# Kernel tuning notes

Measured on AMD Instinct MI355X. Metric: run time of the kernel, lower is better.

Reference implementation:

```python
import jax, jax.numpy as jnp
import numpy as np

B = 65536
A_CH, S_CH, D_CH = 64, 256, 256
IN_CH = A_CH + S_CH + D_CH   # 576
MID = 32
OUT_CH = 4 * S_CH            # 1024
R_IN = IN_CH + S_CH          # 832

def _xavier(key, fan_in, fan_out):
    lim = np.sqrt(6.0 / (fan_in + fan_out)).astype(np.float32)
    return jax.random.uniform(key, (fan_in, fan_out), jnp.float32, -lim, lim)

def setup_inputs() -> dict:
    key = jax.random.key(0)
    ks = jax.random.split(key, 8)
    return {
        "prev_h": jax.random.normal(ks[0], (B, S_CH), jnp.float32),
        "prev_c": jax.random.normal(ks[1], (B, S_CH), jnp.float32),
        "action": jax.random.normal(ks[2], (B, A_CH), jnp.float32),
        "dynamics": jax.random.normal(ks[3], (B, D_CH), jnp.float32),
        "W1": _xavier(ks[4], IN_CH, MID),
        "b1": jnp.zeros((MID,), jnp.float32),
        "W2": _xavier(ks[5], MID, OUT_CH),
        "b2": jnp.zeros((OUT_CH,), jnp.float32),
        "Wr": _xavier(ks[6], R_IN, 1),
        "br": jnp.zeros((1,), jnp.float32),
    }

def reference(prev_h, prev_c, action, dynamics, W1, b1, W2, b2, Wr, br):
    # concat order matches torch: [dynamics, action, prev_h] -> [B, 576]
    x = jnp.concatenate([dynamics, action, prev_h], axis=1)
    h1 = jnp.tanh(x @ W1 + b1)            # fc1: tanh activation, [B, 32]
    g = h1 @ W2 + b2                       # fc2: no activation, [B, 4*S]
    act_i, act_f, hat_c, act_o = jnp.split(g, 4, axis=1)
    act_i = jax.nn.sigmoid(act_i)
    act_f = jax.nn.sigmoid(act_f)
    hat_c = jnp.tanh(hat_c)
    act_o = jax.nn.sigmoid(act_o)
    next_c = act_f * prev_c + act_i * hat_c
    next_h = act_o * jnp.tanh(next_c)
    xr = jnp.concatenate([x, next_h], axis=1)  # [B, 832]
    reward = jnp.tanh(xr @ Wr + br)            # [B, 1]
    return next_h, next_c, reward
```

## Files before the change

### kernel.cpp

```cpp
#include <hip/hip_runtime.h>
#include <hip/hip_bf16.h>

typedef float f32x4 __attribute__((ext_vector_type(4)));
typedef short bf16x8 __attribute__((ext_vector_type(8)));
typedef float float4v __attribute__((ext_vector_type(4)));

#define W2T_OFF (48 * 576)
#define H1_OFF (W2T_OFF + 32 * 1024)

__device__ __forceinline__ short f2bf(float f) {
  __bf16 b = (__bf16)f;
  return __builtin_bit_cast(short, b);
}
__device__ __forceinline__ uint pack2(float a, float b) {
  return (uint)(unsigned short)f2bf(a) | ((uint)(unsigned short)f2bf(b) << 16);
}
__device__ __forceinline__ float fast_sigmoid(float x) {
  return __builtin_amdgcn_rcpf(1.f + __expf(-x));
}
__device__ __forceinline__ float fast_tanh(float x) {
  float e = __expf(2.f * x);
  return 1.f - 2.f * __builtin_amdgcn_rcpf(e + 1.f);
}
__device__ __forceinline__ float4v ld16(const float* p) {
  float4v r;
  asm volatile("global_load_dwordx4 %0, %1, off" : "=v"(r) : "v"(p));
  return r;
}

__global__ __launch_bounds__(256) void prep_weights(
    const float* __restrict__ W1, const float* __restrict__ W2,
    const float* __restrict__ Wr, short* __restrict__ ws)
{
  int i = blockIdx.x * 256 + threadIdx.x;
  if (i < 48 * 576) {
    int n = i / 576;
    int k = i - n * 576;
    float v = 0.f;
    if (n < 32) v = W1[k * 32 + n];
    else if (n == 32) v = Wr[k];
    int phys = n * 576 + ((((k >> 3) ^ (n & 7)) << 3) | (k & 7));
    ws[phys] = f2bf(v);
  } else {
    int j = i - 48 * 576;
    if (j < 32 * 1024) {
      int n = j >> 5;
      int k = j & 31;
      ws[W2T_OFF + j] = f2bf(W2[k * 1024 + n]);
    }
  }
}

__global__ __launch_bounds__(512, 4) void fc1_kernel(
    const float* __restrict__ prev_h, const float* __restrict__ action,
    const float* __restrict__ dynamics, const float* __restrict__ b1,
    const short* __restrict__ wsw, short* __restrict__ h1out,
    float* __restrict__ rdot)
{
  __shared__ short wlds[48 * 576];

  const int t = threadIdx.x;
  #pragma unroll
  for (int i = 0; i < 7; ++i) {
    int off = i * 8192 + t * 16;
    if (off < 55296) {
      __builtin_amdgcn_global_load_lds(
          (const __attribute__((address_space(1))) void*)((const char*)wsw + off),
          (__attribute__((address_space(3))) void*)((char*)wlds + off), 16, 0, 0);
    }
  }
  __syncthreads();

  const int wid = t >> 6, lane = t & 63, lg = lane >> 4, ln = lane & 15;
  const int lnx = ln & 7;
  const int rowA = blockIdx.x * 128 + wid * 16 + ln;
  const int kb = 8 * lg;

  const float* dynp = dynamics + rowA * 256 + kb;
  const float* actp = action   + rowA * 64  + kb;
  const float* hp   = prev_h   + rowA * 256 + kb;

  auto asrc = [&](int j) -> const float* {
    return (j < 8) ? (dynp + 32 * j)
         : (j < 10) ? (actp + 32 * j - 256)
                    : (hp + 32 * j - 320);
  };

  f32x4 acc0 = {0.f,0.f,0.f,0.f};
  f32x4 acc1 = {0.f,0.f,0.f,0.f};
  f32x4 acc2 = {0.f,0.f,0.f,0.f};

  float4v ab[6][2];
  #pragma unroll
  for (int j = 0; j < 6; ++j) {
    const float* p = asrc(j);
    ab[j][0] = ld16(p);
    ab[j][1] = ld16(p + 4);
  }

#define FC1_STEP(J, S, IMM)                                                  \
  {                                                                          \
    asm volatile("s_waitcnt vmcnt(" #IMM ")");                               \
    __builtin_amdgcn_sched_barrier(0);                                       \
    float4v v0 = ab[S][0], v1 = ab[S][1];                                    \
    bf16x8 a;                                                                \
    a[0]=f2bf(v0.x); a[1]=f2bf(v0.y); a[2]=f2bf(v0.z); a[3]=f2bf(v0.w);      \
    a[4]=f2bf(v1.x); a[5]=f2bf(v1.y); a[6]=f2bf(v1.z); a[7]=f2bf(v1.w);      \
    const int uo = ((4 * (J) + lg) ^ lnx) << 3;                              \
    bf16x8 bA = *(const bf16x8*)&wlds[ln * 576 + uo];                        \
    bf16x8 bB = *(const bf16x8*)&wlds[(ln + 16) * 576 + uo];                 \
    bf16x8 bC = *(const bf16x8*)&wlds[(ln + 32) * 576 + uo];                 \
    acc0 = __builtin_amdgcn_mfma_f32_16x16x32_bf16(bA, a, acc0, 0, 0, 0);    \
    acc1 = __builtin_amdgcn_mfma_f32_16x16x32_bf16(bB, a, acc1, 0, 0, 0);    \
    acc2 = __builtin_amdgcn_mfma_f32_16x16x32_bf16(bC, a, acc2, 0, 0, 0);    \
    if ((J) + 6 < 18) {                                                      \
      const float* np = asrc((J) + 6);                                       \
      ab[S][0] = ld16(np);                                                   \
      ab[S][1] = ld16(np + 4);                                               \
    }                                                                        \
  }

  FC1_STEP(0,0,10)  FC1_STEP(1,1,10)  FC1_STEP(2,2,10)  FC1_STEP(3,3,10)
  FC1_STEP(4,4,10)  FC1_STEP(5,5,10)  FC1_STEP(6,0,10)  FC1_STEP(7,1,10)
  FC1_STEP(8,2,10)  FC1_STEP(9,3,10)  FC1_STEP(10,4,10) FC1_STEP(11,5,10)
  FC1_STEP(12,0,10) FC1_STEP(13,1,8)  FC1_STEP(14,2,6)  FC1_STEP(15,3,4)
  FC1_STEP(16,4,2)  FC1_STEP(17,5,0)
#undef FC1_STEP

  float4v b1lo = *(const float4v*)&b1[4 * lg];
  float4v b1hi = *(const float4v*)&b1[16 + 4 * lg];
  uint2 wlo, whi;
  wlo.x = pack2(fast_tanh(acc0[0] + b1lo.x), fast_tanh(acc0[1] + b1lo.y));
  wlo.y = pack2(fast_tanh(acc0[2] + b1lo.z), fast_tanh(acc0[3] + b1lo.w));
  whi.x = pack2(fast_tanh(acc1[0] + b1hi.x), fast_tanh(acc1[1] + b1hi.y));
  whi.y = pack2(fast_tanh(acc1[2] + b1hi.z), fast_tanh(acc1[3] + b1hi.w));
  *(uint2*)&h1out[rowA * 32 + 4 * lg]      = wlo;
  *(uint2*)&h1out[rowA * 32 + 16 + 4 * lg] = whi;
  if (lg == 0) rdot[rowA] = acc2[0];
}

__global__ __launch_bounds__(256, 8) void fc2_kernel(
    const float* __restrict__ prev_c, const float* __restrict__ b2,
    const float* __restrict__ Wr, const float* __restrict__ br,
    const short* __restrict__ wsw, const short* __restrict__ h1in,
    const float* __restrict__ rdot,
    float* __restrict__ out_h, float* __restrict__ out_c, float* __restrict__ out_r)
{
  __shared__ float pc_lds[16 * 256];
  __shared__ float rlds[4][16];

  const int t = threadIdx.x;
  const int ks = t >> 6, lane = t & 63, lg = lane >> 4, ln = lane & 15;
  const int r0 = blockIdx.x * 16;
  const int rowA = r0 + ln;

  {
    const float* src = prev_c + (size_t)r0 * 256;
    #pragma unroll
    for (int i = 0; i < 4; ++i) {
      int u = i * 256 + t;
      int g = (u & ~63) | ((u & 63) ^ ((u >> 6) & 7));
      __builtin_amdgcn_global_load_lds(
          (const __attribute__((address_space(1))) void*)(src + g * 4),
          (__attribute__((address_space(3))) void*)&pc_lds[u * 4], 16, 0, 0);
    }
  }
  bf16x8 af2 = *(const bf16x8*)&h1in[rowA * 32 + 8 * lg];
  __syncthreads();

  float racc = 0.f;
  const float br0 = br[0];
  const short* w2t = wsw + W2T_OFF;
  const size_t orow = (size_t)rowA * 256;
  const int lrow = ln * 64;
  const int lnx = ln & 7;

  auto fc2_tile = [&](int nt, float4v& nh, float4v& nc2) {
    const int c4 = nt * 16 + 4 * lg;
    const short* aw = w2t + (nt * 16 + ln) * 32 + 8 * lg;
    bf16x8 wi = *(const bf16x8*)(aw);
    bf16x8 wf = *(const bf16x8*)(aw + 256 * 32);
    bf16x8 wc = *(const bf16x8*)(aw + 512 * 32);
    bf16x8 wo = *(const bf16x8*)(aw + 768 * 32);
    f32x4 gi = {0.f,0.f,0.f,0.f}, gf = {0.f,0.f,0.f,0.f};
    f32x4 gc = {0.f,0.f,0.f,0.f}, go = {0.f,0.f,0.f,0.f};
    gi = __builtin_amdgcn_mfma_f32_16x16x32_bf16(wi, af2, gi, 0, 0, 0);
    gf = __builtin_amdgcn_mfma_f32_16x16x32_bf16(wf, af2, gf, 0, 0, 0);
    gc = __builtin_amdgcn_mfma_f32_16x16x32_bf16(wc, af2, gc, 0, 0, 0);
    go = __builtin_amdgcn_mfma_f32_16x16x32_bf16(wo, af2, go, 0, 0, 0);
    float4v pc = *(const float4v*)&pc_lds[(lrow + ((nt * 4 + lg) ^ lnx)) * 4];
    float4v b2i = *(const float4v*)&b2[c4];
    float4v b2f = *(const float4v*)&b2[256 + c4];
    float4v b2c = *(const float4v*)&b2[512 + c4];
    float4v b2o = *(const float4v*)&b2[768 + c4];
    float4v wrv = *(const float4v*)&Wr[576 + c4];
    #pragma unroll
    for (int r = 0; r < 4; ++r) {
      float iv  = fast_sigmoid(gi[r] + b2i[r]);
      float fv  = fast_sigmoid(gf[r] + b2f[r]);
      float cv  = fast_tanh(gc[r] + b2c[r]);
      float ov  = fast_sigmoid(go[r] + b2o[r]);
      float ncv = fv * pc[r] + iv * cv;
      float nhv = ov * fast_tanh(ncv);
      nh[r]  = nhv;
      nc2[r] = ncv;
      racc += nhv * wrv[r];
    }
  };

  #pragma unroll
  for (int qq = 0; qq < 2; ++qq) {
    const int nt0 = ks * 4 + 2 * qq;
    float4v nh0, nc0, nh1, nc1;
    fc2_tile(nt0,     nh0, nc0);
    fc2_tile(nt0 + 1, nh1, nc1);
    const size_t b0 = orow + nt0 * 16 + 4 * lg;
    __builtin_nontemporal_store(nh0, (float4v*)(out_h + b0));
    __builtin_nontemporal_store(nh1, (float4v*)(out_h + b0 + 16));
    __builtin_nontemporal_store(nc0, (float4v*)(out_c + b0));
    __builtin_nontemporal_store(nc1, (float4v*)(out_c + b0 + 16));
  }

  racc += __shfl_xor(racc, 16, 64);
  racc += __shfl_xor(racc, 32, 64);
  if (ks > 0 && lane < 16) rlds[ks][lane] = racc;
  asm volatile("s_waitcnt lgkmcnt(0)" ::: "memory");
  __builtin_amdgcn_s_barrier();
  __builtin_amdgcn_sched_barrier(0);
  if (ks == 0 && lg == 0) {
    float s = rdot[rowA] + racc + rlds[1][ln] + rlds[2][ln] + rlds[3][ln] + br0;
    __builtin_nontemporal_store(fast_tanh(s), &out_r[rowA]);
  }
}

extern "C" void kernel_launch(void* const* d_in, const int* in_sizes, int n_in,
                              void* d_out, int out_size, void* d_ws, size_t ws_size,
                              hipStream_t stream) {
  const float* prev_h   = (const float*)d_in[0];
  const float* prev_c   = (const float*)d_in[1];
  const float* action   = (const float*)d_in[2];
  const float* dynamics = (const float*)d_in[3];
  const float* W1 = (const float*)d_in[4];
  const float* b1 = (const float*)d_in[5];
  const float* W2 = (const float*)d_in[6];
  const float* b2 = (const float*)d_in[7];
  const float* Wr = (const float*)d_in[8];
  const float* br = (const float*)d_in[9];

  short* wsw   = (short*)d_ws;
  short* h1buf = wsw + H1_OFF;
  float* rdot  = (float*)(h1buf + (size_t)65536 * 32);

  float* out_h = (float*)d_out;
  float* out_c = out_h + (size_t)65536 * 256;
  float* out_r = out_c + (size_t)65536 * 256;

  prep_weights<<<236, 256, 0, stream>>>(W1, W2, Wr, wsw);
  fc1_kernel<<<512, 512, 0, stream>>>(prev_h, action, dynamics, b1, wsw, h1buf, rdot);
  fc2_kernel<<<4096, 256, 0, stream>>>(prev_c, b2, Wr, br, wsw, h1buf, rdot,
                                       out_h, out_c, out_r);
}
```

Baseline: 78.98 us.

## Fuse fc1 and fc2 LSTM stages into one kernel with pipelined W2/prev_c loads

```diff
diff --git a/kernel.cpp b/kernel.cpp
--- a/kernel.cpp
+++ b/kernel.cpp
@@ -6,7 +6,8 @@
 typedef float float4v __attribute__((ext_vector_type(4)));
 
 #define W2T_OFF (48 * 576)
-#define H1_OFF (W2T_OFF + 32 * 1024)
+#define BIAS_OFF 60416
+#define BIAS_FLOATS 1328
 
 __device__ __forceinline__ short f2bf(float f) {
   __bf16 b = (__bf16)f;
@@ -27,10 +28,17 @@
   asm volatile("global_load_dwordx4 %0, %1, off" : "=v"(r) : "v"(p));
   return r;
 }
+__device__ __forceinline__ bf16x8 ld16w(const short* p) {
+  bf16x8 r;
+  asm volatile("global_load_dwordx4 %0, %1, off" : "=v"(r) : "v"(p));
+  return r;
+}
 
 __global__ __launch_bounds__(256) void prep_weights(
     const float* __restrict__ W1, const float* __restrict__ W2,
-    const float* __restrict__ Wr, short* __restrict__ ws)
+    const float* __restrict__ Wr, const float* __restrict__ b1,
+    const float* __restrict__ b2, const float* __restrict__ br,
+    short* __restrict__ ws)
 {
   int i = blockIdx.x * 256 + threadIdx.x;
   if (i < 48 * 576) {
@@ -41,25 +49,35 @@
     else if (n == 32) v = Wr[k];
     int phys = n * 576 + ((((k >> 3) ^ (n & 7)) << 3) | (k & 7));
     ws[phys] = f2bf(v);
+  } else if (i < BIAS_OFF) {
+    int j = i - 48 * 576;
+    int n = j >> 5, k = j & 31;
+    ws[W2T_OFF + j] = f2bf(W2[k * 1024 + n]);
   } else {
-    int j = i - 48 * 576;
-    if (j < 32 * 1024) {
-      int n = j >> 5;
-      int k = j & 31;
-      ws[W2T_OFF + j] = f2bf(W2[k * 1024 + n]);
+    int i2 = i - BIAS_OFF;
+    if (i2 < BIAS_FLOATS) {
+      float v = 0.f;
+      if (i2 < 1024) v = b2[i2];
+      else if (i2 < 1280) v = Wr[576 + (i2 - 1024)];
+      else if (i2 < 1312) v = b1[i2 - 1280];
+      else if (i2 == 1312) v = br[0];
+      ((float*)(ws + BIAS_OFF))[i2] = v;
     }
   }
 }
 
-__global__ __launch_bounds__(512, 4) void fc1_kernel(
-    const float* __restrict__ prev_h, const float* __restrict__ action,
-    const float* __restrict__ dynamics, const float* __restrict__ b1,
-    const short* __restrict__ wsw, short* __restrict__ h1out,
-    float* __restrict__ rdot)
+__global__ __launch_bounds__(512) void fclstm_fused(
+    const float* __restrict__ prev_h, const float* __restrict__ prev_c,
+    const float* __restrict__ action, const float* __restrict__ dynamics,
+    const short* __restrict__ wsw,
+    float* __restrict__ out_h, float* __restrict__ out_c, float* __restrict__ out_r)
 {
   __shared__ short wlds[48 * 576];
+  __shared__ short h1T[128 * 40];
+  __shared__ float blds[BIAS_FLOATS];
 
   const int t = threadIdx.x;
+
   #pragma unroll
   for (int i = 0; i < 7; ++i) {
     int off = i * 8192 + t * 16;
@@ -69,11 +87,20 @@
           (__attribute__((address_space(3))) void*)((char*)wlds + off), 16, 0, 0);
     }
   }
+  {
+    const float* bsrc = (const float*)(wsw + BIAS_OFF);
+    if (t < BIAS_FLOATS / 4) {
+      __builtin_amdgcn_global_load_lds(
+          (const __attribute__((address_space(1))) void*)(bsrc + t * 4),
+          (__attribute__((address_space(3))) void*)&blds[t * 4], 16, 0, 0);
+    }
+  }
   __syncthreads();
 
   const int wid = t >> 6, lane = t & 63, lg = lane >> 4, ln = lane & 15;
   const int lnx = ln & 7;
-  const int rowA = blockIdx.x * 128 + wid * 16 + ln;
+  const int rowL = wid * 16 + ln;
+  const int rowA = blockIdx.x * 128 + rowL;
   const int kb = 8 * lg;
 
   const float* dynp = dynamics + rowA * 256 + kb;
@@ -127,110 +154,97 @@
   FC1_STEP(16,4,2)  FC1_STEP(17,5,0)
 #undef FC1_STEP
 
-  float4v b1lo = *(const float4v*)&b1[4 * lg];
-  float4v b1hi = *(const float4v*)&b1[16 + 4 * lg];
-  uint2 wlo, whi;
-  wlo.x = pack2(fast_tanh(acc0[0] + b1lo.x), fast_tanh(acc0[1] + b1lo.y));
-  wlo.y = pack2(fast_tanh(acc0[2] + b1lo.z), fast_tanh(acc0[3] + b1lo.w));
-  whi.x = pack2(fast_tanh(acc1[0] + b1hi.x), fast_tanh(acc1[1] + b1hi.y));
-  whi.y = pack2(fast_tanh(acc1[2] + b1hi.z), fast_tanh(acc1[3] + b1hi.w));
-  *(uint2*)&h1out[rowA * 32 + 4 * lg]      = wlo;
-  *(uint2*)&h1out[rowA * 32 + 16 + 4 * lg] = whi;
-  if (lg == 0) rdot[rowA] = acc2[0];
-}
-
-__global__ __launch_bounds__(256, 8) void fc2_kernel(
-    const float* __restrict__ prev_c, const float* __restrict__ b2,
-    const float* __restrict__ Wr, const float* __restrict__ br,
-    const short* __restrict__ wsw, const short* __restrict__ h1in,
-    const float* __restrict__ rdot,
-    float* __restrict__ out_h, float* __restrict__ out_c, float* __restrict__ out_r)
-{
-  __shared__ float pc_lds[16 * 256];
-  __shared__ float rlds[4][16];
-
-  const int t = threadIdx.x;
-  const int ks = t >> 6, lane = t & 63, lg = lane >> 4, ln = lane & 15;
-  const int r0 = blockIdx.x * 16;
-  const int rowA = r0 + ln;
+  const float* pcp = prev_c + (size_t)rowA * 256 + 4 * lg;
+  const short* w2t = wsw + W2T_OFF;
+  float4v pcq[3];
+  bf16x8  Wq[2][4];
+  #pragma unroll
+  for (int q = 0; q < 3; ++q) pcq[q] = ld16(pcp + q * 16);
+  #pragma unroll
+  for (int q = 0; q < 2; ++q) {
+    const short* aw = w2t + (q * 16 + ln) * 32 + 8 * lg;
+    Wq[q][0] = ld16w(aw);
+    Wq[q][1] = ld16w(aw + 256 * 32);
+    Wq[q][2] = ld16w(aw + 512 * 32);
+    Wq[q][3] = ld16w(aw + 768 * 32);
+  }
 
   {
-    const float* src = prev_c + (size_t)r0 * 256;
-    #pragma unroll
-    for (int i = 0; i < 4; ++i) {
-      int u = i * 256 + t;
-      int g = (u & ~63) | ((u & 63) ^ ((u >> 6) & 7));
-      __builtin_amdgcn_global_load_lds(
-          (const __attribute__((address_space(1))) void*)(src + g * 4),
-          (__attribute__((address_space(3))) void*)&pc_lds[u * 4], 16, 0, 0);
-    }
-  }
-  bf16x8 af2 = *(const bf16x8*)&h1in[rowA * 32 + 8 * lg];
-  __syncthreads();
-
+    float4v b1lo = *(const float4v*)&blds[1280 + 4 * lg];
+    float4v b1hi = *(const float4v*)&blds[1280 + 16 + 4 * lg];
+    uint2 wlo, whi;
+    wlo.x = pack2(fast_tanh(acc0[0] + b1lo.x), fast_tanh(acc0[1] + b1lo.y));
+    wlo.y = pack2(fast_tanh(acc0[2] + b1lo.z), fast_tanh(acc0[3] + b1lo.w));
+    whi.x = pack2(fast_tanh(acc1[0] + b1hi.x), fast_tanh(acc1[1] + b1hi.y));
+    whi.y = pack2(fast_tanh(acc1[2] + b1hi.z), fast_tanh(acc1[3] + b1hi.w));
+    short* hrow = &h1T[rowL * 40];
+    *(uint2*)(hrow + 4 * lg)      = wlo;
+    *(uint2*)(hrow + 16 + 4 * lg) = whi;
+  }
+  asm volatile("s_waitcnt lgkmcnt(0)" ::: "memory");
+  __builtin_amdgcn_sched_barrier(0);
+  bf16x8 af2 = *(const bf16x8*)(&h1T[rowL * 40] + 8 * lg);
+
+  const size_t orow = (size_t)rowA * 256;
   float racc = 0.f;
-  const float br0 = br[0];
-  const short* w2t = wsw + W2T_OFF;
-  const size_t orow = (size_t)rowA * 256;
-  const int lrow = ln * 64;
-  const int lnx = ln & 7;
-
-  auto fc2_tile = [&](int nt, float4v& nh, float4v& nc2) {
-    const int c4 = nt * 16 + 4 * lg;
-    const short* aw = w2t + (nt * 16 + ln) * 32 + 8 * lg;
-    bf16x8 wi = *(const bf16x8*)(aw);
-    bf16x8 wf = *(const bf16x8*)(aw + 256 * 32);
-    bf16x8 wc = *(const bf16x8*)(aw + 512 * 32);
-    bf16x8 wo = *(const bf16x8*)(aw + 768 * 32);
-    f32x4 gi = {0.f,0.f,0.f,0.f}, gf = {0.f,0.f,0.f,0.f};
-    f32x4 gc = {0.f,0.f,0.f,0.f}, go = {0.f,0.f,0.f,0.f};
-    gi = __builtin_amdgcn_mfma_f32_16x16x32_bf16(wi, af2, gi, 0, 0, 0);
-    gf = __builtin_amdgcn_mfma_f32_16x16x32_bf16(wf, af2, gf, 0, 0, 0);
-    gc = __builtin_amdgcn_mfma_f32_16x16x32_bf16(wc, af2, gc, 0, 0, 0);
-    go = __builtin_amdgcn_mfma_f32_16x16x32_bf16(wo, af2, go, 0, 0, 0);
-    float4v pc = *(const float4v*)&pc_lds[(lrow + ((nt * 4 + lg) ^ lnx)) * 4];
-    float4v b2i = *(const float4v*)&b2[c4];
-    float4v b2f = *(const float4v*)&b2[256 + c4];
-    float4v b2c = *(const float4v*)&b2[512 + c4];
-    float4v b2o = *(const float4v*)&b2[768 + c4];
-    float4v wrv = *(const float4v*)&Wr[576 + c4];
-    #pragma unroll
-    for (int r = 0; r < 4; ++r) {
-      float iv  = fast_sigmoid(gi[r] + b2i[r]);
-      float fv  = fast_sigmoid(gf[r] + b2f[r]);
-      float cv  = fast_tanh(gc[r] + b2c[r]);
-      float ov  = fast_sigmoid(go[r] + b2o[r]);
-      float ncv = fv * pc[r] + iv * cv;
-      float nhv = ov * fast_tanh(ncv);
-      nh[r]  = nhv;
-      nc2[r] = ncv;
-      racc += nhv * wrv[r];
-    }
-  };
-
-  #pragma unroll
-  for (int qq = 0; qq < 2; ++qq) {
-    const int nt0 = ks * 4 + 2 * qq;
-    float4v nh0, nc0, nh1, nc1;
-    fc2_tile(nt0,     nh0, nc0);
-    fc2_tile(nt0 + 1, nh1, nc1);
-    const size_t b0 = orow + nt0 * 16 + 4 * lg;
-    __builtin_nontemporal_store(nh0, (float4v*)(out_h + b0));
-    __builtin_nontemporal_store(nh1, (float4v*)(out_h + b0 + 16));
-    __builtin_nontemporal_store(nc0, (float4v*)(out_c + b0));
-    __builtin_nontemporal_store(nc1, (float4v*)(out_c + b0 + 16));
-  }
+
+#define FC2_TILE(T, VM)                                                       \
+  {                                                                           \
+    asm volatile("s_waitcnt vmcnt(" #VM ")");                                 \
+    __builtin_amdgcn_sched_barrier(0);                                        \
+    f32x4 gi = {0.f,0.f,0.f,0.f}, gf = {0.f,0.f,0.f,0.f};                     \
+    f32x4 gc = {0.f,0.f,0.f,0.f}, go = {0.f,0.f,0.f,0.f};                     \
+    gi = __builtin_amdgcn_mfma_f32_16x16x32_bf16(Wq[(T)&1][0], af2, gi,0,0,0);\
+    gf = __builtin_amdgcn_mfma_f32_16x16x32_bf16(Wq[(T)&1][1], af2, gf,0,0,0);\
+    gc = __builtin_amdgcn_mfma_f32_16x16x32_bf16(Wq[(T)&1][2], af2, gc,0,0,0);\
+    go = __builtin_amdgcn_mfma_f32_16x16x32_bf16(Wq[(T)&1][3], af2, go,0,0,0);\
+    float4v pcv = pcq[(T) % 3];                                               \
+    const int c4 = (T) * 16 + 4 * lg;                                         \
+    float4v b2i = *(const float4v*)&blds[c4];                                 \
+    float4v b2f = *(const float4v*)&blds[256 + c4];                           \
+    float4v b2c = *(const float4v*)&blds[512 + c4];                           \
+    float4v b2o = *(const float4v*)&blds[768 + c4];                           \
+    float4v wrv = *(const float4v*)&blds[1024 + c4];                          \
+    float4v nh, nc2;                                                          \
+    _Pragma("unroll")                                                         \
+    for (int r = 0; r < 4; ++r) {                                             \
+      float iv  = fast_sigmoid(gi[r] + b2i[r]);                               \
+      float fv  = fast_sigmoid(gf[r] + b2f[r]);                               \
+      float cv  = fast_tanh(gc[r] + b2c[r]);                                  \
+      float ov  = fast_sigmoid(go[r] + b2o[r]);                               \
+      float ncv = fv * pcv[r] + iv * cv;                                      \
+      float nhv = ov * fast_tanh(ncv);                                        \
+      nh[r]  = nhv;                                                           \
+      nc2[r] = ncv;                                                           \
+      racc += nhv * wrv[r];                                                   \
+    }                                                                         \
+    __builtin_nontemporal_store(nh,  (float4v*)(out_h + orow + c4));          \
+    __builtin_nontemporal_store(nc2, (float4v*)(out_c + orow + c4));          \
+    if ((T) + 3 <= 15) {         \
+      pcq[(T) % 3] = ld16(pcp + ((T) + 3) * 16);                              \
+    }                                                                         \
+    if ((T) + 2 <= 15) {                                                      \
+      const short* awn = w2t + ((((T) + 2) * 16 + ln)) * 32 + 8 * lg;         \
+      Wq[(T)&1][0] = ld16w(awn);                                              \
+      Wq[(T)&1][1] = ld16w(awn + 256 * 32);                                   \
+      Wq[(T)&1][2] = ld16w(awn + 512 * 32);                                   \
+      Wq[(T)&1][3] = ld16w(awn + 768 * 32);                                   \
+    }                                                                         \
+  }
+
+  FC2_TILE(0,4)   FC2_TILE(1,5)   FC2_TILE(2,5)   FC2_TILE(3,5)
+  FC2_TILE(4,5)   FC2_TILE(5,5)   FC2_TILE(6,5)   FC2_TILE(7,5)
+  FC2_TILE(8,5)   FC2_TILE(9,5)   FC2_TILE(10,5)  FC2_TILE(11,5)
+  FC2_TILE(12,5)  FC2_TILE(13,5)  FC2_TILE(14,4)  FC2_TILE(15,0)
+#undef FC2_TILE
 
   racc += __shfl_xor(racc, 16, 64);
   racc += __shfl_xor(racc, 32, 64);
-  if (ks > 0 && lane < 16) rlds[ks][lane] = racc;
-  asm volatile("s_waitcnt lgkmcnt(0)" ::: "memory");
-  __builtin_amdgcn_s_barrier();
-  __builtin_amdgcn_sched_barrier(0);
-  if (ks == 0 && lg == 0) {
-    float s = rdot[rowA] + racc + rlds[1][ln] + rlds[2][ln] + rlds[3][ln] + br0;
+  if (lg == 0) {
+    float s = acc2[0] + racc + blds[1312];
     __builtin_nontemporal_store(fast_tanh(s), &out_r[rowA]);
   }
+  asm volatile("s_waitcnt vmcnt(0)");
 }
 
 extern "C" void kernel_launch(void* const* d_in, const int* in_sizes, int n_in,
@@ -247,16 +261,13 @@
   const float* Wr = (const float*)d_in[8];
   const float* br = (const float*)d_in[9];
 
-  short* wsw   = (short*)d_ws;
-  short* h1buf = wsw + H1_OFF;
-  float* rdot  = (float*)(h1buf + (size_t)65536 * 32);
+  short* wsw = (short*)d_ws;
 
   float* out_h = (float*)d_out;
   float* out_c = out_h + (size_t)65536 * 256;
   float* out_r = out_c + (size_t)65536 * 256;
 
-  prep_weights<<<236, 256, 0, stream>>>(W1, W2, Wr, wsw);
-  fc1_kernel<<<512, 512, 0, stream>>>(prev_h, action, dynamics, b1, wsw, h1buf, rdot);
-  fc2_kernel<<<4096, 256, 0, stream>>>(prev_c, b2, Wr, br, wsw, h1buf, rdot,
-                                       out_h, out_c, out_r);
-}
+  prep_weights<<<242, 256, 0, stream>>>(W1, W2, Wr, b1, b2, br, wsw);
+  fclstm_fused<<<512, 512, 0, stream>>>(prev_h, prev_c, action, dynamics,
+                                        wsw, out_h, out_c, out_r);
+}
```

Measured after the change: 69.45 us (median of 2 runs). 1.14x faster.
